# Optimization experiments

Measured on AMD Instinct MI355X. Metric: run time of the kernel, lower is better.

Reference implementation:

```python
import jax, jax.numpy as jnp
import numpy as np

EMBED_DIM = 64       # embedding_dim (latent channels)
NUM_ATOMS = 1024     # num_embeddings (dictionary atoms)
SPARSITY = 8         # sparsity_level
N_PIXELS = 16384     # flattened latent pixels (e.g. B=16, 32x32 grid)
DIAG_EPS = 1e-4
CHOL_EPS = 1e-6


def setup_inputs() -> dict:
    key = jax.random.key(0)
    kx, kd = jax.random.split(key)
    X = jax.random.normal(kx, (EMBED_DIM, N_PIXELS), dtype=jnp.float32)
    # dictionary parameter initialized as randn * 0.02, per the module __init__
    D = jax.random.normal(kd, (EMBED_DIM, NUM_ATOMS), dtype=jnp.float32) * 0.02
    return {"X": X, "D": D}


def _nan0(x):
    return jnp.nan_to_num(x, nan=0.0, posinf=0.0, neginf=0.0)


def _batched_omp(X, D, sparsity_level):
    """Batched OMP with sequential Cholesky updates.

    X: [d, N] signals, D: [d, K] dictionary.
    Returns (I [N, S] int32 support indices, coeffs [N, S] ordered coefficients).
    """
    X = _nan0(X)
    D = _nan0(D)
    d, n = X.shape
    k = D.shape[1]
    rows = jnp.arange(n)

    G = D.T @ D + DIAG_EPS * jnp.eye(k, dtype=D.dtype)   # [K, K] Gram
    h_bar = (D.T @ X).T                                   # [N, K] correlations
    h = h_bar
    mask = jnp.zeros((n, k), dtype=bool)                  # selected-atom mask
    L = None                                              # batched Cholesky [N, s, s]
    I = jnp.zeros((n, 0), dtype=jnp.int32)
    coeffs = jnp.zeros((n, 0), dtype=X.dtype)

    for s in range(sparsity_level):  # static unroll, S is small
        scores = jnp.where(mask, jnp.asarray(-1.0, X.dtype), jnp.abs(h))
        idx = jnp.argmax(scores, axis=1)                  # [N]
        mask = mask.at[rows, idx].set(True)
        diag_g = G[idx, idx][:, None, None]               # [N, 1, 1]
        if s == 0:
            L = jnp.sqrt(jnp.clip(diag_g, CHOL_EPS))      # [N, 1, 1]
        else:
            # G[I[n, j], idx[n]] for each batch element n -> [N, s, 1]
            G_col = G[I, idx[:, None]][..., None]
            w = jax.scipy.linalg.solve_triangular(L, G_col, lower=True)  # [N, s, 1]
            wt = jnp.swapaxes(w, 1, 2)                                   # [N, 1, s]
            corner = jnp.sqrt(jnp.clip(diag_g - jnp.sum(w * w, axis=1, keepdims=True), CHOL_EPS))
            zeros_col = jnp.zeros((n, s, 1), dtype=X.dtype)
            L = jnp.concatenate(
                [jnp.concatenate([L, zeros_col], axis=2),
                 jnp.concatenate([wt, corner], axis=2)], axis=1)          # [N, s+1, s+1]
        I = jnp.concatenate([I, idx[:, None].astype(jnp.int32)], axis=1)  # [N, s+1]
        # solve (L L^T) x = h_bar[support] via two triangular solves (cholesky_solve)
        h_stack = jnp.take_along_axis(h_bar, I, axis=1)[..., None]        # [N, s+1, 1]
        y = jax.scipy.linalg.solve_triangular(L, h_stack, lower=True)
        x_stack = jax.scipy.linalg.solve_triangular(jnp.swapaxes(L, 1, 2), y, lower=False)
        coeffs = _nan0(x_stack[..., 0])                                   # [N, s+1]
        # beta = coeffs @ G[support, :]  -> residual correlation update
        beta = jnp.einsum('ns,nsk->nk', coeffs, G[I])
        h = _nan0(h_bar - beta)
    return I, coeffs


def reference(X, D):
    I, coeffs = _batched_omp(X, D, SPARSITY)
    atoms = D[:, I]                                  # [d, N, S]
    recon = jnp.einsum('ns,dns->nd', coeffs, atoms)  # [N, d] sparse reconstruction
    return recon, I, coeffs
```

## Files before the change

kernel.cpp:

```cpp
#include <hip/hip_runtime.h>
#include <cmath>

#define NPIX 16384
#define NATOM 1024
#define DIM 64
#define SPAR 8

__global__ __launch_bounds__(256) void k_pre(const float* __restrict__ X,
                                             const float* __restrict__ D,
                                             float* __restrict__ G,
                                             float* __restrict__ Dt,
                                             float* __restrict__ Gd,
                                             float* __restrict__ HB) {
  __shared__ float smem[2 * DIM * 128];
  const int b = blockIdx.x;
  if (b < 256) {
    const int i0 = (b >> 4) * 64, j0 = (b & 15) * 64;
    float(*sA)[65] = (float(*)[65])smem;
    float(*sB)[65] = (float(*)[65])(smem + DIM * 65);
    for (int t = threadIdx.x; t < DIM * 16; t += 256) {
      int d = t >> 4, c4 = (t & 15) * 4;
      *reinterpret_cast<float4*>(&sA[d][c4]) =
          *reinterpret_cast<const float4*>(&D[(size_t)d * NATOM + i0 + c4]);
      *reinterpret_cast<float4*>(&sB[d][c4]) =
          *reinterpret_cast<const float4*>(&D[(size_t)d * NATOM + j0 + c4]);
    }
    __syncthreads();
    const int ty = (threadIdx.x >> 4) * 4;
    const int tx = (threadIdx.x & 15) * 4;
    double acc[4][4];
#pragma unroll
    for (int ii = 0; ii < 4; ++ii)
#pragma unroll
      for (int jj = 0; jj < 4; ++jj) acc[ii][jj] = 0.0;
    for (int d = 0; d < DIM; ++d) {
      float a[4], bb[4];
#pragma unroll
      for (int ii = 0; ii < 4; ++ii) a[ii] = sA[d][ty + ii];
#pragma unroll
      for (int jj = 0; jj < 4; ++jj) bb[jj] = sB[d][tx + jj];
#pragma unroll
      for (int ii = 0; ii < 4; ++ii)
#pragma unroll
        for (int jj = 0; jj < 4; ++jj)
          acc[ii][jj] += (double)a[ii] * (double)bb[jj];
    }
#pragma unroll
    for (int ii = 0; ii < 4; ++ii)
#pragma unroll
      for (int jj = 0; jj < 4; ++jj) {
        const int k1 = i0 + ty + ii, k2 = j0 + tx + jj;
        float g = (float)acc[ii][jj];
        if (k1 == k2) {
          g += 1e-4f;
          Gd[k1] = g;
        }
        G[(size_t)k1 * NATOM + k2] = g;
      }
  } else if (b < 320) {
    const int base = (b - 256) * 1024 + threadIdx.x * 4;
    float4 v = *reinterpret_cast<const float4*>(&D[base]);
    const float vv[4] = {v.x, v.y, v.z, v.w};
#pragma unroll
    for (int e = 0; e < 4; ++e) {
      int idx = base + e;
      Dt[(size_t)(idx & (NATOM - 1)) * DIM + (idx >> 10)] = vv[e];
    }
  } else {
    const int bx = b - 320;
    const int n0 = (bx & 127) * 128, k0 = (bx >> 7) * 128;
    float(*sX)[128] = (float(*)[128])smem;
    float(*sD)[128] = (float(*)[128])(smem + DIM * 128);
    for (int i = threadIdx.x; i < DIM * 32; i += 256) {
      int d = i >> 5, c4 = (i & 31) * 4;
      *reinterpret_cast<float4*>(&sX[d][c4]) =
          *reinterpret_cast<const float4*>(&X[(size_t)d * NPIX + n0 + c4]);
      *reinterpret_cast<float4*>(&sD[d][c4]) =
          *reinterpret_cast<const float4*>(&D[(size_t)d * NATOM + k0 + c4]);
    }
    __syncthreads();
    const int nl = (threadIdx.x & 15) * 8;
    const int kl = (threadIdx.x >> 4) * 8;
    float acc[8][8];
#pragma unroll
    for (int i = 0; i < 8; ++i)
#pragma unroll
      for (int j = 0; j < 8; ++j) acc[i][j] = 0.f;
#pragma unroll 4
    for (int d = 0; d < DIM; ++d) {
      float xv[8], dv[8];
      *reinterpret_cast<float4*>(&xv[0]) = *reinterpret_cast<float4*>(&sX[d][nl]);
      *reinterpret_cast<float4*>(&xv[4]) = *reinterpret_cast<float4*>(&sX[d][nl + 4]);
      *reinterpret_cast<float4*>(&dv[0]) = *reinterpret_cast<float4*>(&sD[d][kl]);
      *reinterpret_cast<float4*>(&dv[4]) = *reinterpret_cast<float4*>(&sD[d][kl + 4]);
#pragma unroll
      for (int i = 0; i < 8; ++i)
#pragma unroll
        for (int j = 0; j < 8; ++j) acc[i][j] = fmaf(xv[i], dv[j], acc[i][j]);
    }
#pragma unroll
    for (int i = 0; i < 8; ++i)
#pragma unroll
      for (int j = 0; j < 2; ++j)
        *reinterpret_cast<float4*>(
            &HB[(size_t)(n0 + nl + i) * NATOM + k0 + kl + j * 4]) =
            *reinterpret_cast<float4*>(&acc[i][j * 4]);
  }
}

template <int CTRL>
__device__ __forceinline__ float dpp_fmax(float x) {
  int s = __builtin_amdgcn_update_dpp(__float_as_int(x), __float_as_int(x),
                                      CTRL, 0xf, 0xf, false);
  return fmaxf(x, __int_as_float(s));
}
__device__ __forceinline__ float wave_max_bcast(float x) {
  x = dpp_fmax<0x111>(x);
  x = dpp_fmax<0x112>(x);
  x = dpp_fmax<0x114>(x);
  x = dpp_fmax<0x118>(x);
  x = dpp_fmax<0x142>(x);
  x = dpp_fmax<0x143>(x);
  return __int_as_float(__builtin_amdgcn_readlane(__float_as_int(x), 63));
}

__global__ __launch_bounds__(128, 3) void k_omp2(const float* __restrict__ HB,
                                                 const float* __restrict__ Dt,
                                                 const float* __restrict__ G,
                                                 const float* __restrict__ Gd,
                                                 float* __restrict__ out) {
  const int lane = threadIdx.x & 63;
  const int wave = threadIdx.x >> 6;
  const int kbase = wave * 512 + lane * 8;
  const int n = __builtin_amdgcn_readfirstlane(blockIdx.x);

  __shared__ float sM[2][2];
  __shared__ int sC[2][2];

  float hb[8];
#pragma unroll
  for (int q = 0; q < 2; ++q) {
    float4 v = *reinterpret_cast<const float4*>(
        &HB[(size_t)n * NATOM + kbase + q * 4]);
    hb[q * 4 + 0] = v.x; hb[q * 4 + 1] = v.y;
    hb[q * 4 + 2] = v.z; hb[q * 4 + 3] = v.w;
  }
#pragma unroll
  for (int j = 0; j < 8; ++j) asm volatile("" : "+v"(hb[j]));

  int selI[SPAR];
  float rows[SPAR - 1][8];
  float Lm[SPAR][SPAR], invL[SPAR], ysel[SPAR], coefF[SPAR];

#pragma unroll 8
  for (int s = 0; s < SPAR; ++s) {
    float h[8];
#pragma unroll
    for (int j = 0; j < 8; ++j) {
      float hv = hb[j];
#pragma unroll
      for (int i = 0; i < SPAR - 1; ++i)
        if (i < s) hv = fmaf(-coefF[i], rows[i][j], hv);
      h[j] = hv;
    }
    float ml = fmaxf(fmaxf(fmaxf(fabsf(h[0]), fabsf(h[1])), fabsf(h[2])), fabsf(h[3]));
    float mh = fmaxf(fmaxf(fmaxf(fabsf(h[4]), fabsf(h[5])), fabsf(h[6])), fabsf(h[7]));
    const float Mw = wave_max_bcast(fmaxf(ml, mh));
    unsigned cand = NATOM;
#pragma unroll
    for (int j = 7; j >= 0; --j)
      cand = (fabsf(h[j]) == Mw) ? (unsigned)(kbase + j) : cand;
    unsigned long long bal = __ballot(cand != (unsigned)NATOM);
    const int fl = __ffsll(bal) - 1;
    const int cw = __builtin_amdgcn_readlane((int)cand, fl);
    if (lane == 0) {
      sM[s & 1][wave] = Mw;
      sC[s & 1][wave] = cw;
    }
    __syncthreads();
    const float M0 = sM[s & 1][0], M1 = sM[s & 1][1];
    const int c0 = sC[s & 1][0], c1 = sC[s & 1][1];
    int bkv;
    if (M0 > M1) bkv = c0;
    else if (M1 > M0) bkv = c1;
    else bkv = c0 < c1 ? c0 : c1;
    const int bk = __builtin_amdgcn_readfirstlane(bkv);
    selI[s] = bk;

    const float hbs = HB[(size_t)n * NATOM + bk];

    if ((bk >> 9) == wave && lane == ((bk >> 3) & 63)) {
#pragma unroll
      for (int j = 0; j < 8; ++j)
        if (j == (bk & 7)) hb[j] = __builtin_nanf("");
    }

    if (s < SPAR - 1) {
#pragma unroll
      for (int q = 0; q < 2; ++q) {
        float4 rv = *reinterpret_cast<const float4*>(
            &G[(size_t)bk * NATOM + kbase + q * 4]);
        rows[s][q * 4 + 0] = rv.x; rows[s][q * 4 + 1] = rv.y;
        rows[s][q * 4 + 2] = rv.z; rows[s][q * 4 + 3] = rv.w;
      }
    }

    const float diag = Gd[bk];
    float w[SPAR];
    float sq = 0.f;
#pragma unroll
    for (int i = 0; i < SPAR; ++i)
      if (i < s) {
        float a = G[(size_t)selI[i] * NATOM + bk];
#pragma unroll
        for (int t = 0; t < SPAR; ++t)
          if (t < i) a = fmaf(-Lm[i][t], w[t], a);
        w[i] = a * invL[i];
        sq += w[i] * w[i];
        Lm[s][i] = w[i];
      }
    float cc = diag - sq;
    if (cc < 1e-6f) cc = 1e-6f;
    invL[s] = 1.0f / sqrtf(cc);

    {
      float a = hbs;
#pragma unroll
      for (int t = 0; t < SPAR; ++t)
        if (t < s) a = fmaf(-Lm[s][t], ysel[t], a);
      ysel[s] = a * invL[s];
    }
#pragma unroll
    for (int i = SPAR - 1; i >= 0; --i)
      if (i <= s) {
        float a = ysel[i];
#pragma unroll
        for (int t = 0; t < SPAR; ++t)
          if (t > i && t <= s) a = fmaf(-Lm[t][i], coefF[t], a);
        coefF[i] = a * invL[i];
      }

    if (s < SPAR - 1) {
#pragma unroll
      for (int j = 0; j < 8; ++j) asm volatile("" : "+v"(rows[s][j]));
    }
  }

  if (wave == 0) {
    double r = 0.0;
#pragma unroll
    for (int i = 0; i < SPAR; ++i)
      r += (double)coefF[i] * (double)Dt[(size_t)selI[i] * DIM + lane];
    out[(size_t)n * DIM + lane] = (float)r;
  } else {
    float fi = 0.f, fc = 0.f;
#pragma unroll
    for (int i = 0; i < SPAR; ++i)
      if (lane == i) { fi = (float)selI[i]; fc = coefF[i]; }
    if (lane < SPAR) {
      out[(size_t)NPIX * DIM + (size_t)n * SPAR + lane] = fi;
      out[(size_t)NPIX * DIM + (size_t)NPIX * SPAR + (size_t)n * SPAR + lane] = fc;
    }
  }
}

__global__ __launch_bounds__(64) void k_omp_fb(const float* __restrict__ X,
                                               const float* __restrict__ D,
                                               const float* __restrict__ G,
                                               const float* __restrict__ Gd,
                                               float* __restrict__ out) {
  const int lane = threadIdx.x & 63;
  const int lane16 = lane * 16;
  const int n = __builtin_amdgcn_readfirstlane(blockIdx.x);

  float hb[16];
  {
    double a[16];
#pragma unroll
    for (int j = 0; j < 16; ++j) a[j] = 0.0;
    for (int d = 0; d < DIM; ++d) {
      float xd = X[(size_t)d * NPIX + n];
#pragma unroll
      for (int j = 0; j < 16; ++j)
        a[j] += (double)xd * (double)D[(size_t)d * NATOM + lane16 + j];
    }
#pragma unroll
    for (int j = 0; j < 16; ++j) hb[j] = (float)a[j];
  }
#pragma unroll
  for (int j = 0; j < 16; ++j) asm volatile("" : "+v"(hb[j]));

  int selI[SPAR];
  float rows[SPAR - 1][16];
  float Lm[SPAR][SPAR], invL[SPAR], ysel[SPAR], coefF[SPAR];

#pragma unroll 8
  for (int s = 0; s < SPAR; ++s) {
    float h[16];
#pragma unroll
    for (int j = 0; j < 16; ++j) {
      float hv = hb[j];
#pragma unroll
      for (int i = 0; i < SPAR - 1; ++i)
        if (i < s) hv = fmaf(-coefF[i], rows[i][j], hv);
      h[j] = hv;
    }
    float m0 = fmaxf(fmaxf(fmaxf(fabsf(h[0]), fabsf(h[1])), fabsf(h[2])), fabsf(h[3]));
    float m1 = fmaxf(fmaxf(fmaxf(fabsf(h[4]), fabsf(h[5])), fabsf(h[6])), fabsf(h[7]));
    float m2 = fmaxf(fmaxf(fmaxf(fabsf(h[8]), fabsf(h[9])), fabsf(h[10])), fabsf(h[11]));
    float m3 = fmaxf(fmaxf(fmaxf(fabsf(h[12]), fabsf(h[13])), fabsf(h[14])), fabsf(h[15]));
    const float M = wave_max_bcast(fmaxf(fmaxf(m0, m1), fmaxf(m2, m3)));
    unsigned cand = NATOM;
#pragma unroll
    for (int j = 15; j >= 0; --j)
      cand = (fabsf(h[j]) == M) ? (unsigned)(lane16 + j) : cand;
    unsigned long long bal = __ballot(cand != (unsigned)NATOM);
    const int fl = __ffsll(bal) - 1;
    const int bk = __builtin_amdgcn_readlane((int)cand, fl);
    selI[s] = bk;
    const int bl = bk >> 4, bj = bk & 15;

    float v = 0.f;
#pragma unroll
    for (int j = 0; j < 16; ++j)
      if (j == bj) v = hb[j];
    const float hbs =
        __int_as_float(__builtin_amdgcn_readlane(__float_as_int(v), bl));

#pragma unroll
    for (int j = 0; j < 16; ++j)
      if (j == bj && lane == bl) hb[j] = __builtin_nanf("");

    if (s < SPAR - 1) {
#pragma unroll
      for (int q = 0; q < 4; ++q) {
        float4 rv = *reinterpret_cast<const float4*>(
            &G[(size_t)bk * NATOM + lane16 + q * 4]);
        rows[s][q * 4 + 0] = rv.x; rows[s][q * 4 + 1] = rv.y;
        rows[s][q * 4 + 2] = rv.z; rows[s][q * 4 + 3] = rv.w;
      }
    }

    const float diag = Gd[bk];
    float w[SPAR];
    float sq = 0.f;
#pragma unroll
    for (int i = 0; i < SPAR; ++i)
      if (i < s) {
        float a = G[(size_t)selI[i] * NATOM + bk];
#pragma unroll
        for (int t = 0; t < SPAR; ++t)
          if (t < i) a = fmaf(-Lm[i][t], w[t], a);
        w[i] = a * invL[i];
        sq += w[i] * w[i];
        Lm[s][i] = w[i];
      }
    float cc = diag - sq;
    if (cc < 1e-6f) cc = 1e-6f;
    invL[s] = 1.0f / sqrtf(cc);
    {
      float a = hbs;
#pragma unroll
      for (int t = 0; t < SPAR; ++t)
        if (t < s) a = fmaf(-Lm[s][t], ysel[t], a);
      ysel[s] = a * invL[s];
    }
#pragma unroll
    for (int i = SPAR - 1; i >= 0; --i)
      if (i <= s) {
        float a = ysel[i];
#pragma unroll
        for (int t = 0; t < SPAR; ++t)
          if (t > i && t <= s) a = fmaf(-Lm[t][i], coefF[t], a);
        coefF[i] = a * invL[i];
      }
    if (s < SPAR - 1) {
#pragma unroll
      for (int j = 0; j < 16; ++j) asm volatile("" : "+v"(rows[s][j]));
    }
  }

  double r = 0.0;
#pragma unroll
  for (int i = 0; i < SPAR; ++i)
    r += (double)coefF[i] * (double)D[(size_t)lane * NATOM + selI[i]];
  out[(size_t)n * DIM + lane] = (float)r;

  float fi = 0.f, fc = 0.f;
#pragma unroll
  for (int i = 0; i < SPAR; ++i)
    if (lane == i) { fi = (float)selI[i]; fc = coefF[i]; }
  if (lane < SPAR) {
    out[(size_t)NPIX * DIM + (size_t)n * SPAR + lane] = fi;
    out[(size_t)NPIX * DIM + (size_t)NPIX * SPAR + (size_t)n * SPAR + lane] = fc;
  }
}

__global__ __launch_bounds__(256) void k_gram(const float* __restrict__ D,
                                              float* __restrict__ G,
                                              float* __restrict__ Gd) {
  int k1 = blockIdx.x;
  __shared__ float d1[DIM];
  if (threadIdx.x < DIM) d1[threadIdx.x] = D[(size_t)threadIdx.x * NATOM + k1];
  __syncthreads();
  for (int k2 = threadIdx.x; k2 < NATOM; k2 += 256) {
    double acc = 0.0;
#pragma unroll
    for (int d = 0; d < DIM; ++d)
      acc += (double)d1[d] * (double)D[(size_t)d * NATOM + k2];
    float g = (float)acc;
    if (k2 == k1) {
      g += 1e-4f;
      Gd[k1] = g;
    }
    G[(size_t)k1 * NATOM + k2] = g;
  }
}

extern "C" void kernel_launch(void* const* d_in, const int* in_sizes, int n_in,
                              void* d_out, int out_size, void* d_ws,
                              size_t ws_size, hipStream_t stream) {
  const float* X = (const float*)d_in[0];
  const float* D = (const float*)d_in[1];
  float* out = (float*)d_out;
  float* G = (float*)d_ws;
  float* Dt = G + (size_t)NATOM * NATOM;
  float* Gd = Dt + (size_t)NATOM * DIM;
  float* HB = Gd + NATOM;
  const size_t needFull =
      ((size_t)NATOM * NATOM + (size_t)NATOM * DIM + NATOM +
       (size_t)NPIX * NATOM) * sizeof(float);

  if (ws_size >= needFull) {
    k_pre<<<dim3(1344), dim3(256), 0, stream>>>(X, D, G, Dt, Gd, HB);
    k_omp2<<<dim3(NPIX), dim3(128), 0, stream>>>(HB, Dt, G, Gd, out);
  } else {
    k_gram<<<dim3(NATOM), dim3(256), 0, stream>>>(D, G, Gd);
    k_omp_fb<<<dim3(NPIX), dim3(64), 0, stream>>>(X, D, G, Gd, out);
  }
}
```

Measured before the change: 112.7 us.

## Use single-wave OMP with incremental orthogonalized residual updates

Replaces the two-wave-per-pixel OMP kernel with a one-wave-per-pixel kernel, which removes the shared-memory exchange and __syncthreads in each argmax step. The residual correlation is now updated with one orthogonalized Gram row per step (a forward-substituted L^{-1}G row scaled by y_s) instead of re-solving all coefficients and applying every stored Gram row. The back-substitution for the coefficients runs only once at the end. In exchange each lane holds 16 atoms and 7x16 stored rows, which raises register pressure and may reduce occupancy, and the altered floating-point order could change argmax tie-breaking.

```diff
diff --git a/kernel.cpp b/kernel.cpp
--- a/kernel.cpp
+++ b/kernel.cpp
@@ -124,94 +124,93 @@
   return __int_as_float(__builtin_amdgcn_readlane(__float_as_int(x), 63));
 }
 
-__global__ __launch_bounds__(128, 3) void k_omp2(const float* __restrict__ HB,
-                                                 const float* __restrict__ Dt,
-                                                 const float* __restrict__ G,
-                                                 const float* __restrict__ Gd,
-                                                 float* __restrict__ out) {
+template <bool HBWS, bool DTW>
+__global__ __launch_bounds__(64) void k_omp(const float* __restrict__ HB,
+                                            const float* __restrict__ X,
+                                            const float* __restrict__ D,
+                                            const float* __restrict__ Dt,
+                                            const float* __restrict__ G,
+                                            const float* __restrict__ Gd,
+                                            float* __restrict__ out) {
   const int lane = threadIdx.x & 63;
-  const int wave = threadIdx.x >> 6;
-  const int kbase = wave * 512 + lane * 8;
+  const int lane16 = lane * 16;
   const int n = __builtin_amdgcn_readfirstlane(blockIdx.x);
 
-  __shared__ float sM[2][2];
-  __shared__ int sC[2][2];
-
-  float hb[8];
-#pragma unroll
-  for (int q = 0; q < 2; ++q) {
-    float4 v = *reinterpret_cast<const float4*>(
-        &HB[(size_t)n * NATOM + kbase + q * 4]);
-    hb[q * 4 + 0] = v.x; hb[q * 4 + 1] = v.y;
-    hb[q * 4 + 2] = v.z; hb[q * 4 + 3] = v.w;
-  }
-#pragma unroll
-  for (int j = 0; j < 8; ++j) asm volatile("" : "+v"(hb[j]));
+  float h[16];
+  if (HBWS) {
+#pragma unroll
+    for (int q = 0; q < 4; ++q) {
+      float4 v = *reinterpret_cast<const float4*>(
+          &HB[(size_t)n * NATOM + lane16 + q * 4]);
+      h[q * 4 + 0] = v.x; h[q * 4 + 1] = v.y;
+      h[q * 4 + 2] = v.z; h[q * 4 + 3] = v.w;
+    }
+  } else {
+    double a[16];
+#pragma unroll
+    for (int j = 0; j < 16; ++j) a[j] = 0.0;
+    for (int d = 0; d < DIM; ++d) {
+      float xd = X[(size_t)d * NPIX + n];
+#pragma unroll
+      for (int j = 0; j < 16; ++j)
+        a[j] += (double)xd * (double)D[(size_t)d * NATOM + lane16 + j];
+    }
+#pragma unroll
+    for (int j = 0; j < 16; ++j) h[j] = (float)a[j];
+  }
+#pragma unroll
+  for (int j = 0; j < 16; ++j) asm volatile("" : "+v"(h[j]));
 
   int selI[SPAR];
-  float rows[SPAR - 1][8];
-  float Lm[SPAR][SPAR], invL[SPAR], ysel[SPAR], coefF[SPAR];
+  float wr[SPAR - 1][16];
+  float hbsel[SPAR];
+  float Lm[SPAR][SPAR], invL[SPAR], ysel[SPAR];
 
 #pragma unroll 8
   for (int s = 0; s < SPAR; ++s) {
-    float h[8];
-#pragma unroll
-    for (int j = 0; j < 8; ++j) {
-      float hv = hb[j];
-#pragma unroll
-      for (int i = 0; i < SPAR - 1; ++i)
-        if (i < s) hv = fmaf(-coefF[i], rows[i][j], hv);
-      h[j] = hv;
-    }
-    float ml = fmaxf(fmaxf(fmaxf(fabsf(h[0]), fabsf(h[1])), fabsf(h[2])), fabsf(h[3]));
-    float mh = fmaxf(fmaxf(fmaxf(fabsf(h[4]), fabsf(h[5])), fabsf(h[6])), fabsf(h[7]));
-    const float Mw = wave_max_bcast(fmaxf(ml, mh));
+    float m0 = fmaxf(fmaxf(fabsf(h[0]), fabsf(h[1])), fmaxf(fabsf(h[2]), fabsf(h[3])));
+    float m1 = fmaxf(fmaxf(fabsf(h[4]), fabsf(h[5])), fmaxf(fabsf(h[6]), fabsf(h[7])));
+    float m2 = fmaxf(fmaxf(fabsf(h[8]), fabsf(h[9])), fmaxf(fabsf(h[10]), fabsf(h[11])));
+    float m3 = fmaxf(fmaxf(fabsf(h[12]), fabsf(h[13])), fmaxf(fabsf(h[14]), fabsf(h[15])));
+    const float M = wave_max_bcast(fmaxf(fmaxf(m0, m1), fmaxf(m2, m3)));
     unsigned cand = NATOM;
 #pragma unroll
-    for (int j = 7; j >= 0; --j)
-      cand = (fabsf(h[j]) == Mw) ? (unsigned)(kbase + j) : cand;
+    for (int j = 15; j >= 0; --j)
+      cand = (fabsf(h[j]) == M) ? (unsigned)(lane16 + j) : cand;
     unsigned long long bal = __ballot(cand != (unsigned)NATOM);
     const int fl = __ffsll(bal) - 1;
-    const int cw = __builtin_amdgcn_readlane((int)cand, fl);
-    if (lane == 0) {
-      sM[s & 1][wave] = Mw;
-      sC[s & 1][wave] = cw;
-    }
-    __syncthreads();
-    const float M0 = sM[s & 1][0], M1 = sM[s & 1][1];
-    const int c0 = sC[s & 1][0], c1 = sC[s & 1][1];
-    int bkv;
-    if (M0 > M1) bkv = c0;
-    else if (M1 > M0) bkv = c1;
-    else bkv = c0 < c1 ? c0 : c1;
-    const int bk = __builtin_amdgcn_readfirstlane(bkv);
+    const int bk = __builtin_amdgcn_readlane((int)cand, fl);
     selI[s] = bk;
-
-    const float hbs = HB[(size_t)n * NATOM + bk];
-
-    if ((bk >> 9) == wave && lane == ((bk >> 3) & 63)) {
-#pragma unroll
-      for (int j = 0; j < 8; ++j)
-        if (j == (bk & 7)) hb[j] = __builtin_nanf("");
-    }
-
+    const int bl = bk >> 4, bj = bk & 15;
+
+#pragma unroll
+    for (int j = 0; j < 16; ++j)
+      if (j == bj && lane == bl) h[j] = __builtin_nanf("");
+
+    float g[16];
     if (s < SPAR - 1) {
 #pragma unroll
-      for (int q = 0; q < 2; ++q) {
+      for (int q = 0; q < 4; ++q) {
         float4 rv = *reinterpret_cast<const float4*>(
-            &G[(size_t)bk * NATOM + kbase + q * 4]);
-        rows[s][q * 4 + 0] = rv.x; rows[s][q * 4 + 1] = rv.y;
-        rows[s][q * 4 + 2] = rv.z; rows[s][q * 4 + 3] = rv.w;
-      }
-    }
-
+            &G[(size_t)bk * NATOM + lane16 + q * 4]);
+        g[q * 4 + 0] = rv.x; g[q * 4 + 1] = rv.y;
+        g[q * 4 + 2] = rv.z; g[q * 4 + 3] = rv.w;
+      }
+    }
+
+    const float hbs = HB ? HB[(size_t)n * NATOM + bk] : 0.f;
+    hbsel[s] = hbs;
     const float diag = Gd[bk];
+    float colv[SPAR];
+#pragma unroll
+    for (int i = 0; i < SPAR; ++i)
+      if (i < s) colv[i] = G[(size_t)selI[i] * NATOM + bk];
     float w[SPAR];
     float sq = 0.f;
 #pragma unroll
     for (int i = 0; i < SPAR; ++i)
       if (i < s) {
-        float a = G[(size_t)selI[i] * NATOM + bk];
+        float a = colv[i];
 #pragma unroll
         for (int t = 0; t < SPAR; ++t)
           if (t < i) a = fmaf(-Lm[i][t], w[t], a);
@@ -230,37 +229,49 @@
         if (t < s) a = fmaf(-Lm[s][t], ysel[t], a);
       ysel[s] = a * invL[s];
     }
-#pragma unroll
-    for (int i = SPAR - 1; i >= 0; --i)
-      if (i <= s) {
-        float a = ysel[i];
-#pragma unroll
-        for (int t = 0; t < SPAR; ++t)
-          if (t > i && t <= s) a = fmaf(-Lm[t][i], coefF[t], a);
-        coefF[i] = a * invL[i];
-      }
 
     if (s < SPAR - 1) {
 #pragma unroll
-      for (int j = 0; j < 8; ++j) asm volatile("" : "+v"(rows[s][j]));
-    }
-  }
-
-  if (wave == 0) {
-    double r = 0.0;
-#pragma unroll
-    for (int i = 0; i < SPAR; ++i)
-      r += (double)coefF[i] * (double)Dt[(size_t)selI[i] * DIM + lane];
-    out[(size_t)n * DIM + lane] = (float)r;
-  } else {
-    float fi = 0.f, fc = 0.f;
-#pragma unroll
-    for (int i = 0; i < SPAR; ++i)
-      if (lane == i) { fi = (float)selI[i]; fc = coefF[i]; }
-    if (lane < SPAR) {
-      out[(size_t)NPIX * DIM + (size_t)n * SPAR + lane] = fi;
-      out[(size_t)NPIX * DIM + (size_t)NPIX * SPAR + (size_t)n * SPAR + lane] = fc;
-    }
+      for (int j = 0; j < 16; ++j) {
+        float a = g[j];
+#pragma unroll
+        for (int t = 0; t < SPAR - 1; ++t)
+          if (t < s) a = fmaf(-Lm[s][t], wr[t][j], a);
+        float v = a * invL[s];
+        wr[s][j] = v;
+        h[j] = fmaf(-ysel[s], v, h[j]);
+      }
+#pragma unroll
+      for (int j = 0; j < 16; ++j) asm volatile("" : "+v"(wr[s][j]));
+    }
+  }
+
+  float coefF[SPAR];
+#pragma unroll
+  for (int i = SPAR - 1; i >= 0; --i) {
+    float a = ysel[i];
+#pragma unroll
+    for (int t = 0; t < SPAR; ++t)
+      if (t > i) a = fmaf(-Lm[t][i], coefF[t], a);
+    coefF[i] = a * invL[i];
+  }
+
+  double r = 0.0;
+#pragma unroll
+  for (int i = 0; i < SPAR; ++i) {
+    float dv = DTW ? Dt[(size_t)selI[i] * DIM + lane]
+                   : D[(size_t)lane * NATOM + selI[i]];
+    r += (double)coefF[i] * (double)dv;
+  }
+  out[(size_t)n * DIM + lane] = (float)r;
+
+  float fi = 0.f, fc = 0.f;
+#pragma unroll
+  for (int i = 0; i < SPAR; ++i)
+    if (lane == i) { fi = (float)selI[i]; fc = coefF[i]; }
+  if (lane < SPAR) {
+    out[(size_t)NPIX * DIM + (size_t)n * SPAR + lane] = fi;
+    out[(size_t)NPIX * DIM + (size_t)NPIX * SPAR + (size_t)n * SPAR + lane] = fc;
   }
 }
 
@@ -433,7 +444,8 @@
 
   if (ws_size >= needFull) {
     k_pre<<<dim3(1344), dim3(256), 0, stream>>>(X, D, G, Dt, Gd, HB);
-    k_omp2<<<dim3(NPIX), dim3(128), 0, stream>>>(HB, Dt, G, Gd, out);
+    k_omp<true, true><<<dim3(NPIX), dim3(64), 0, stream>>>(
+        HB, X, D, Dt, G, Gd, out);
   } else {
     k_gram<<<dim3(NATOM), dim3(256), 0, stream>>>(D, G, Gd);
     k_omp_fb<<<dim3(NPIX), dim3(64), 0, stream>>>(X, D, G, Gd, out);
```

After: 100.3 us. 1.12x faster.

## Update residual correlations incrementally via Cholesky-whitened Gram rows

Applied to the files above, without the earlier changes.

Replaces the per-iteration recomputation of h = hb - sum coef_i * G_row_i with an incremental update: each new Gram row is whitened by the current Cholesky factor (wr) and h is reduced by ysel[s]*wr[s]. The back-substitution for coefficients moves out of the loop and runs once at the end. Scalar Cholesky quantities are forced into SGPRs with readfirstlane, and the column loads are batched before use. This cuts the per-iteration FMA count and the serial back-solve in exchange for a triangular forward pass over the stored rows and some floating-point reordering.

```diff
diff --git a/kernel.cpp b/kernel.cpp
--- a/kernel.cpp
+++ b/kernel.cpp
@@ -124,6 +124,10 @@
   return __int_as_float(__builtin_amdgcn_readlane(__float_as_int(x), 63));
 }
 
+__device__ __forceinline__ float sgprf(float x) {
+  return __int_as_float(__builtin_amdgcn_readfirstlane(__float_as_int(x)));
+}
+
 __global__ __launch_bounds__(128, 3) void k_omp2(const float* __restrict__ HB,
                                                  const float* __restrict__ Dt,
                                                  const float* __restrict__ G,
@@ -137,39 +141,33 @@
   __shared__ float sM[2][2];
   __shared__ int sC[2][2];
 
-  float hb[8];
+  float h[8];
 #pragma unroll
   for (int q = 0; q < 2; ++q) {
     float4 v = *reinterpret_cast<const float4*>(
         &HB[(size_t)n * NATOM + kbase + q * 4]);
-    hb[q * 4 + 0] = v.x; hb[q * 4 + 1] = v.y;
-    hb[q * 4 + 2] = v.z; hb[q * 4 + 3] = v.w;
-  }
-#pragma unroll
-  for (int j = 0; j < 8; ++j) asm volatile("" : "+v"(hb[j]));
+    h[q * 4 + 0] = v.x; h[q * 4 + 1] = v.y;
+    h[q * 4 + 2] = v.z; h[q * 4 + 3] = v.w;
+  }
+#pragma unroll
+  for (int j = 0; j < 8; ++j) asm volatile("" : "+v"(h[j]));
 
   int selI[SPAR];
-  float rows[SPAR - 1][8];
-  float Lm[SPAR][SPAR], invL[SPAR], ysel[SPAR], coefF[SPAR];
+  float wr[SPAR - 1][8];
+  float Lm[SPAR][SPAR], invL[SPAR], ysel[SPAR];
 
 #pragma unroll 8
   for (int s = 0; s < SPAR; ++s) {
-    float h[8];
-#pragma unroll
-    for (int j = 0; j < 8; ++j) {
-      float hv = hb[j];
-#pragma unroll
-      for (int i = 0; i < SPAR - 1; ++i)
-        if (i < s) hv = fmaf(-coefF[i], rows[i][j], hv);
-      h[j] = hv;
-    }
-    float ml = fmaxf(fmaxf(fmaxf(fabsf(h[0]), fabsf(h[1])), fabsf(h[2])), fabsf(h[3]));
-    float mh = fmaxf(fmaxf(fmaxf(fabsf(h[4]), fabsf(h[5])), fabsf(h[6])), fabsf(h[7]));
+    float ml = fmaxf(fmaxf(fabsf(h[0]), fabsf(h[1])), fmaxf(fabsf(h[2]), fabsf(h[3])));
+    float mh = fmaxf(fmaxf(fabsf(h[4]), fabsf(h[5])), fmaxf(fabsf(h[6]), fabsf(h[7])));
     const float Mw = wave_max_bcast(fmaxf(ml, mh));
-    unsigned cand = NATOM;
-#pragma unroll
-    for (int j = 7; j >= 0; --j)
-      cand = (fabsf(h[j]) == Mw) ? (unsigned)(kbase + j) : cand;
+    unsigned c0 = NATOM, c1 = NATOM;
+#pragma unroll
+    for (int j = 3; j >= 0; --j) {
+      c0 = (fabsf(h[j]) == Mw) ? (unsigned)(kbase + j) : c0;
+      c1 = (fabsf(h[4 + j]) == Mw) ? (unsigned)(kbase + 4 + j) : c1;
+    }
+    unsigned cand = c0 < c1 ? c0 : c1;
     unsigned long long bal = __ballot(cand != (unsigned)NATOM);
     const int fl = __ffsll(bal) - 1;
     const int cw = __builtin_amdgcn_readlane((int)cand, fl);
@@ -179,71 +177,85 @@
     }
     __syncthreads();
     const float M0 = sM[s & 1][0], M1 = sM[s & 1][1];
-    const int c0 = sC[s & 1][0], c1 = sC[s & 1][1];
+    const int cc0 = sC[s & 1][0], cc1 = sC[s & 1][1];
     int bkv;
-    if (M0 > M1) bkv = c0;
-    else if (M1 > M0) bkv = c1;
-    else bkv = c0 < c1 ? c0 : c1;
+    if (M0 > M1) bkv = cc0;
+    else if (M1 > M0) bkv = cc1;
+    else bkv = cc0 < cc1 ? cc0 : cc1;
     const int bk = __builtin_amdgcn_readfirstlane(bkv);
     selI[s] = bk;
 
-    const float hbs = HB[(size_t)n * NATOM + bk];
-
     if ((bk >> 9) == wave && lane == ((bk >> 3) & 63)) {
 #pragma unroll
       for (int j = 0; j < 8; ++j)
-        if (j == (bk & 7)) hb[j] = __builtin_nanf("");
-    }
-
+        if (j == (bk & 7)) h[j] = __builtin_nanf("");
+    }
+
+    float g[8];
     if (s < SPAR - 1) {
 #pragma unroll
       for (int q = 0; q < 2; ++q) {
         float4 rv = *reinterpret_cast<const float4*>(
             &G[(size_t)bk * NATOM + kbase + q * 4]);
-        rows[s][q * 4 + 0] = rv.x; rows[s][q * 4 + 1] = rv.y;
-        rows[s][q * 4 + 2] = rv.z; rows[s][q * 4 + 3] = rv.w;
-      }
-    }
-
+        g[q * 4 + 0] = rv.x; g[q * 4 + 1] = rv.y;
+        g[q * 4 + 2] = rv.z; g[q * 4 + 3] = rv.w;
+      }
+    }
+
+    const float hbs = HB[(size_t)n * NATOM + bk];
     const float diag = Gd[bk];
+    float colv[SPAR];
+#pragma unroll
+    for (int i = 0; i < SPAR; ++i)
+      if (i < s) colv[i] = G[(size_t)selI[i] * NATOM + bk];
     float w[SPAR];
     float sq = 0.f;
 #pragma unroll
     for (int i = 0; i < SPAR; ++i)
       if (i < s) {
-        float a = G[(size_t)selI[i] * NATOM + bk];
+        float a = colv[i];
 #pragma unroll
         for (int t = 0; t < SPAR; ++t)
           if (t < i) a = fmaf(-Lm[i][t], w[t], a);
         w[i] = a * invL[i];
         sq += w[i] * w[i];
-        Lm[s][i] = w[i];
+        Lm[s][i] = sgprf(w[i]);
       }
     float cc = diag - sq;
     if (cc < 1e-6f) cc = 1e-6f;
-    invL[s] = 1.0f / sqrtf(cc);
-
+    invL[s] = sgprf(1.0f / sqrtf(cc));
     {
       float a = hbs;
 #pragma unroll
       for (int t = 0; t < SPAR; ++t)
         if (t < s) a = fmaf(-Lm[s][t], ysel[t], a);
-      ysel[s] = a * invL[s];
-    }
-#pragma unroll
-    for (int i = SPAR - 1; i >= 0; --i)
-      if (i <= s) {
-        float a = ysel[i];
-#pragma unroll
-        for (int t = 0; t < SPAR; ++t)
-          if (t > i && t <= s) a = fmaf(-Lm[t][i], coefF[t], a);
-        coefF[i] = a * invL[i];
-      }
+      ysel[s] = sgprf(a * invL[s]);
+    }
 
     if (s < SPAR - 1) {
 #pragma unroll
-      for (int j = 0; j < 8; ++j) asm volatile("" : "+v"(rows[s][j]));
-    }
+      for (int j = 0; j < 8; ++j) {
+        float a = g[j];
+#pragma unroll
+        for (int t = 0; t < SPAR - 1; ++t)
+          if (t < s) a = fmaf(-Lm[s][t], wr[t][j], a);
+        float v = a * invL[s];
+        wr[s][j] = v;
+        h[j] = fmaf(-ysel[s], v, h[j]);
+      }
+#pragma unroll
+      for (int j = 0; j < 8; ++j) asm volatile("" : "+v"(wr[s][j]));
+    }
+  }
+
+  float coefF[SPAR];
+#pragma unroll
+  for (int i = SPAR - 1; i >= 0; --i) {
+    float a = ysel[i];
+#pragma unroll
+    for (int t = 0; t < SPAR; ++t)
+      if (t > i) a = fmaf(-Lm[t][i], coefF[t], a);
+    coefF[i] = a * invL[i];
   }
 
   if (wave == 0) {
```

After: 114.9 us. 2.0% more time.
